# Kernel optimization log

Measured on AMD Instinct MI355X. Metric: run time of the kernel, lower is better.

Reference implementation:

```python
import math
import jax, jax.numpy as jnp
import numpy as np

V, D, H, L, F, T, B = 32000, 1024, 16, 4, 4096, 1024, 2
HD = D // H
EPS = 1e-5


def make_pe(max_len, d):
    pos = np.arange(max_len)[:, None].astype(np.float32)
    div = np.exp(np.arange(0, d, 2).astype(np.float32) * (-math.log(10000.0) / d))
    pe = np.zeros((max_len, d), dtype=np.float32)
    pe[:, 0::2] = np.sin(pos * div)
    pe[:, 1::2] = np.cos(pos * div)
    return jnp.asarray(pe)


def setup_inputs() -> dict:
    key = jax.random.key(0)
    ks = jax.random.split(key, 12)
    s = 0.02
    inp = {
        'tokens': jax.random.randint(ks[0], (B, T), 0, V, dtype=jnp.int32),
        'mask': jnp.tril(jnp.ones((T, T), dtype=jnp.int32)),
        'emb': jax.random.normal(ks[1], (V, D), jnp.float32) * s,
        'pe': make_pe(T, D),
        'ln1_g': jnp.ones((L, D)), 'ln1_b': jnp.zeros((L, D)),
        'Wqkv': jax.random.normal(ks[2], (L, D, 3 * D), jnp.float32) * s,
        'bqkv': jnp.zeros((L, 3 * D)),
        'Wproj': jax.random.normal(ks[3], (L, D, D), jnp.float32) * s,
        'bproj': jnp.zeros((L, D)),
        'ln2_g': jnp.ones((L, D)), 'ln2_b': jnp.zeros((L, D)),
        'W1': jax.random.normal(ks[4], (L, D, F), jnp.float32) * s,
        'b1': jnp.zeros((L, F)),
        'W2': jax.random.normal(ks[5], (L, F, D), jnp.float32) * s,
        'b2': jnp.zeros((L, D)),
        'lnf_g': jnp.ones((D,)), 'lnf_b': jnp.zeros((D,)),
        'out_b': jnp.zeros((V,)),
    }
    return inp


def layer_norm(x, g, b):
    m = jnp.mean(x, axis=-1, keepdims=True)
    v = jnp.mean((x - m) ** 2, axis=-1, keepdims=True)
    return (x - m) / jnp.sqrt(v + EPS) * g + b


def attention(x, mask, Wqkv, bqkv, Wproj, bproj):
    b, t, c = x.shape
    qkv = (x @ Wqkv + bqkv).reshape(b, t, 3, H, HD)
    q, k, v = jnp.moveaxis(qkv, 2, 0)  # each [B,T,H,HD]
    q = q.transpose(0, 2, 1, 3)  # [B,H,T,HD]
    k = k.transpose(0, 2, 1, 3)
    v = v.transpose(0, 2, 1, 3)
    scores = jnp.einsum('bhqd,bhkd->bhqk', q, k) / math.sqrt(HD)
    scores = jnp.where(mask[None, None] == 0, -1e9, scores)
    attn = jax.nn.softmax(scores, axis=-1)
    out = jnp.einsum('bhqk,bhkd->bhqd', attn, v)
    out = out.transpose(0, 2, 1, 3).reshape(b, t, c)
    return out @ Wproj + bproj, attn


def reference(tokens, mask, emb, pe, ln1_g, ln1_b, Wqkv, bqkv, Wproj, bproj,
              ln2_g, ln2_b, W1, b1, W2, b2, lnf_g, lnf_b, out_b):
    x = emb[tokens] + pe[:tokens.shape[1]]
    attn = None
    for i in range(L):
        a, attn = attention(layer_norm(x, ln1_g[i], ln1_b[i]), mask,
                            Wqkv[i], bqkv[i], Wproj[i], bproj[i])
        x = x + a
        h = layer_norm(x, ln2_g[i], ln2_b[i])
        h = jax.nn.gelu(h @ W1[i] + b1[i], approximate=False) @ W2[i] + b2[i]
        x = x + h
    x = layer_norm(x, lnf_g, lnf_b)
    logits = x @ emb.T + out_b  # weight tying
    return logits, attn
```

## Files before the change

kernel.cpp:

```cpp
#include <hip/hip_runtime.h>
#include <cstdint>

#define DEV static __device__ __forceinline__

typedef unsigned short u16;
typedef __bf16 bf16x8 __attribute__((ext_vector_type(8)));
typedef float f32x4 __attribute__((ext_vector_type(4)));
typedef unsigned short u16x4 __attribute__((ext_vector_type(4)));

constexpr int V = 32000, D = 1024, H = 16, L = 4, F = 4096, T = 1024, B = 2;
constexpr int HD = 64;

DEV u16 f2bf(float f) {
    union { float f; uint32_t i; } c; c.f = f;
    uint32_t x = c.i;
    return (u16)((x + 0x7fffu + ((x >> 16) & 1u)) >> 16);
}
DEV bf16x8 ld8(const u16* p) { return *reinterpret_cast<const bf16x8*>(p); }

DEV void gl16(const void* g, void* l) {
    __builtin_amdgcn_global_load_lds((const __attribute__((address_space(1))) void*)g,
                                     (__attribute__((address_space(3))) void*)l, 16, 0, 0);
}

__global__ __launch_bounds__(256) void k_embln(const int* __restrict__ tok,
        const float* __restrict__ emb, const float* __restrict__ pe,
        const float* __restrict__ g, const float* __restrict__ b,
        float* __restrict__ x, u16* __restrict__ out) {
    int row = blockIdx.x, tid = threadIdx.x;
    int t = row & (T - 1);
    int vv = tok[row];
    f32x4 v = ((const f32x4*)(emb + (size_t)vv * D))[tid] + ((const f32x4*)(pe + (size_t)t * D))[tid];
    ((f32x4*)(x + (size_t)row * D))[tid] = v;
    float s = v[0] + v[1] + v[2] + v[3];
    float s2 = v[0]*v[0] + v[1]*v[1] + v[2]*v[2] + v[3]*v[3];
#pragma unroll
    for (int m = 1; m < 64; m <<= 1) { s += __shfl_xor(s, m); s2 += __shfl_xor(s2, m); }
    __shared__ float ps[4], ps2[4];
    int wave = tid >> 6;
    if ((tid & 63) == 0) { ps[wave] = s; ps2[wave] = s2; }
    __syncthreads();
    s = ps[0] + ps[1] + ps[2] + ps[3];
    s2 = ps2[0] + ps2[1] + ps2[2] + ps2[3];
    float mean = s * (1.f / D);
    float var = s2 * (1.f / D) - mean * mean;
    float r = rsqrtf(var + 1e-5f);
    f32x4 gg = ((const f32x4*)g)[tid];
    f32x4 bb = ((const f32x4*)b)[tid];
    u16x4 o;
#pragma unroll
    for (int j = 0; j < 4; j++) o[j] = f2bf((v[j] - mean) * r * gg[j] + bb[j]);
    ((u16x4*)(out + (size_t)row * D))[tid] = o;
}

template <int S>
__global__ __launch_bounds__(256) void k_redln(const float* __restrict__ pp,
        const float* __restrict__ bias, float* __restrict__ x,
        const float* __restrict__ g, const float* __restrict__ b,
        u16* __restrict__ out) {
    int row = blockIdx.x, tid = threadIdx.x;
    f32x4 v = ((const f32x4*)(x + (size_t)row * D))[tid];
#pragma unroll
    for (int s = 0; s < S; s++)
        v += ((const f32x4*)(pp + ((size_t)s * (B * T) + row) * D))[tid];
    v += ((const f32x4*)bias)[tid];
    ((f32x4*)(x + (size_t)row * D))[tid] = v;
    float s = v[0] + v[1] + v[2] + v[3];
    float s2 = v[0]*v[0] + v[1]*v[1] + v[2]*v[2] + v[3]*v[3];
#pragma unroll
    for (int m = 1; m < 64; m <<= 1) { s += __shfl_xor(s, m); s2 += __shfl_xor(s2, m); }
    __shared__ float ps[4], ps2[4];
    int wave = tid >> 6;
    if ((tid & 63) == 0) { ps[wave] = s; ps2[wave] = s2; }
    __syncthreads();
    s = ps[0] + ps[1] + ps[2] + ps[3];
    s2 = ps2[0] + ps2[1] + ps2[2] + ps2[3];
    float mean = s * (1.f / D);
    float var = s2 * (1.f / D) - mean * mean;
    float r = rsqrtf(var + 1e-5f);
    f32x4 gg = ((const f32x4*)g)[tid];
    f32x4 bb = ((const f32x4*)b)[tid];
    u16x4 o;
#pragma unroll
    for (int j = 0; j < 4; j++) o[j] = f2bf((v[j] - mean) * r * gg[j] + bb[j]);
    ((u16x4*)(out + (size_t)row * D))[tid] = o;
}

__global__ __launch_bounds__(256) void k_cast(const float* __restrict__ src,
        u16* __restrict__ dst) {
    int i = (blockIdx.x * 256 + threadIdx.x) * 4;
    f32x4 v = *(const f32x4*)(src + i);
    u16x4 o;
#pragma unroll
    for (int j = 0; j < 4; j++) o[j] = f2bf(v[j]);
    *(u16x4*)(dst + i) = o;
}

__global__ __launch_bounds__(256) void k_castT4(const float* __restrict__ Wqkv,
        const float* __restrict__ Wproj, const float* __restrict__ W1,
        const float* __restrict__ W2, u16* __restrict__ wt) {
    int bid = blockIdx.x;
    const float* src; u16* dst; int Rr, Cc, t;
    if (bid < 3072)      { src = Wqkv;  dst = wt;                   Rr = D; Cc = 3 * D; t = bid; }
    else if (bid < 4096) { src = Wproj; dst = wt + 3 * D * D;       Rr = D; Cc = D;     t = bid - 3072; }
    else if (bid < 8192) { src = W1;    dst = wt + 4 * D * D;       Rr = D; Cc = F;     t = bid - 4096; }
    else                 { src = W2;    dst = wt + 4 * D * D + D * F; Rr = F; Cc = D;   t = bid - 8192; }
    int ntx = Cc >> 5;
    int c0 = (t % ntx) * 32, r0 = (t / ntx) * 32;
    __shared__ u16 tl[32][33];
    int x = threadIdx.x & 31, y = threadIdx.x >> 5;
#pragma unroll
    for (int i = 0; i < 4; i++)
        tl[y + i * 8][x] = f2bf(src[(size_t)(r0 + y + i * 8) * Cc + c0 + x]);
    __syncthreads();
#pragma unroll
    for (int i = 0; i < 4; i++)
        dst[(size_t)(c0 + y + i * 8) * Rr + r0 + x] = tl[x][y + i * 8];
}

template <int EPI, bool VT>
__global__ __launch_bounds__(256) void k_gemm_bt(
        const u16* __restrict__ A, int lda,
        const u16* __restrict__ Bt, int ldb,
        const float* __restrict__ bias,
        void* __restrict__ Cv, int ldc, int K, u16* __restrict__ vT) {
    __shared__ u16 tA[2][128 * 32];
    __shared__ u16 tB[2][128 * 32];
    int gm = gridDim.x;
    int nwg = gm * gridDim.y;
    int orig = blockIdx.y * gm + blockIdx.x;
    int xcd = orig & 7, idx = orig >> 3;
    int q = nwg >> 3, rr = nwg & 7;
    int wg = (xcd < rr ? xcd * (q + 1) : rr * (q + 1) + (xcd - rr) * q) + idx;
    int m0 = (wg % gm) * 128, n0 = (wg / gm) * 128;
    int koff = (EPI == 4) ? blockIdx.z * K : 0;
    int tid = threadIdx.x, wave = tid >> 6, lane = tid & 63;
    int llo = lane & 15, lhi = lane >> 4;
    int wr = wave >> 1, wc = wave & 1;
    f32x4 acc[4][4] = {};
    int nk = K / 32;
    for (int c = wave; c < 8; c += 4) {
        int e = (c * 64 + lane) * 8;
        int row = e >> 5, col = e & 31;
        gl16(A  + (size_t)(m0 + row) * lda + koff + col, &tA[0][c * 512]);
        gl16(Bt + (size_t)(n0 + row) * ldb + koff + col, &tB[0][c * 512]);
    }
    __syncthreads();
    int cur = 0;
    for (int t = 0; t < nk; ++t) {
        if (t + 1 < nk) {
            int kk = koff + (t + 1) * 32;
            for (int c = wave; c < 8; c += 4) {
                int e = (c * 64 + lane) * 8;
                int row = e >> 5, col = e & 31;
                gl16(A  + (size_t)(m0 + row) * lda + kk + col, &tA[cur ^ 1][c * 512]);
                gl16(Bt + (size_t)(n0 + row) * ldb + kk + col, &tB[cur ^ 1][c * 512]);
            }
        }
        bf16x8 af[4], bfr[4];
#pragma unroll
        for (int mi = 0; mi < 4; mi++) af[mi] = ld8(&tA[cur][(wr * 64 + mi * 16 + llo) * 32 + lhi * 8]);
#pragma unroll
        for (int ni = 0; ni < 4; ni++) bfr[ni] = ld8(&tB[cur][(wc * 64 + ni * 16 + llo) * 32 + lhi * 8]);
#pragma unroll
        for (int mi = 0; mi < 4; mi++)
#pragma unroll
            for (int ni = 0; ni < 4; ni++)
                acc[mi][ni] = __builtin_amdgcn_mfma_f32_16x16x32_bf16(af[mi], bfr[ni], acc[mi][ni], 0, 0, 0);
        __syncthreads();
        cur ^= 1;
    }
#pragma unroll
    for (int ni = 0; ni < 4; ni++) {
        int col = n0 + wc * 64 + ni * 16 + llo;
        float bb = 0.f;
        if (EPI != 4) bb = bias[col];
#pragma unroll
        for (int mi = 0; mi < 4; mi++) {
            int row0 = m0 + wr * 64 + mi * 16 + lhi * 4;
            if (VT && col >= 2 * D) {
                int dv = col - 2 * D;
                int b_ = row0 >> 10, t_ = row0 & (T - 1);
                u16x4 pk;
#pragma unroll
                for (int r = 0; r < 4; r++) pk[r] = f2bf(acc[mi][ni][r] + bb);
                *(u16x4*)(vT + ((size_t)(b_ * 16 + (dv >> 6)) * HD + (dv & 63)) * T + t_) = pk;
            } else {
#pragma unroll
                for (int r = 0; r < 4; r++) {
                    int row = row0 + r;
                    float o = acc[mi][ni][r] + bb;
                    if (EPI == 1) o = 0.5f * o * (1.f + erff(o * 0.70710678118f));
                    if (EPI == 3) {
                        ((float*)Cv)[(size_t)row * ldc + col] = o;
                    } else if (EPI == 4) {
                        ((float*)Cv)[((size_t)blockIdx.z * (B * T) + row) * ldc + col] = o;
                    } else {
                        ((u16*)Cv)[(size_t)row * ldc + col] = f2bf(o);
                    }
                }
            }
        }
    }
}

template <int PW>
__global__ __launch_bounds__(256) void k_fattn(const u16* __restrict__ qkv,
        const u16* __restrict__ vT, u16* __restrict__ out, float* __restrict__ attnF) {
    __shared__ u16 plds[4][16 * 40];
    int bh = blockIdx.y; int b = bh >> 4, h = bh & 15;
    int tid = threadIdx.x, wave = tid >> 6, lane = tid & 63;
    int llo = lane & 15, lhi = lane >> 4;
    int i0 = blockIdx.x * 64 + wave * 16;
    const u16* qb = qkv + (size_t)b * T * (3 * D) + h * HD;
    const u16* kb = qb + D;
    const u16* vt = vT + (size_t)bh * HD * T;
    bf16x8 q0 = ld8(qb + (size_t)(i0 + llo) * (3 * D) + lhi * 8);
    bf16x8 q1 = ld8(qb + (size_t)(i0 + llo) * (3 * D) + 32 + lhi * 8);
    int qrow = i0 + llo;
    float m = -3e38f, s = 0.f;
    f32x4 oacc[4] = {};
    u16* pw = &plds[wave][0];
    for (int k0 = 0; k0 < i0 + 16; k0 += 32) {
        f32x4 sc0 = {}, sc1 = {};
        {
            bf16x8 kf0 = ld8(kb + (size_t)(k0 + llo) * (3 * D) + lhi * 8);
            bf16x8 kf1 = ld8(kb + (size_t)(k0 + llo) * (3 * D) + 32 + lhi * 8);
            sc0 = __builtin_amdgcn_mfma_f32_16x16x32_bf16(kf0, q0, sc0, 0, 0, 0);
            sc0 = __builtin_amdgcn_mfma_f32_16x16x32_bf16(kf1, q1, sc0, 0, 0, 0);
        }
        if (k0 + 16 < i0 + 16) {
            bf16x8 kf0 = ld8(kb + (size_t)(k0 + 16 + llo) * (3 * D) + lhi * 8);
            bf16x8 kf1 = ld8(kb + (size_t)(k0 + 16 + llo) * (3 * D) + 32 + lhi * 8);
            sc1 = __builtin_amdgcn_mfma_f32_16x16x32_bf16(kf0, q0, sc1, 0, 0, 0);
            sc1 = __builtin_amdgcn_mfma_f32_16x16x32_bf16(kf1, q1, sc1, 0, 0, 0);
        }
        float vv[8]; float mx = m;
#pragma unroll
        for (int hf = 0; hf < 2; hf++)
#pragma unroll
            for (int r = 0; r < 4; r++) {
                int k = k0 + hf * 16 + lhi * 4 + r;
                float x = (hf ? sc1[r] : sc0[r]) * 0.125f;
                float v = (k <= qrow) ? x : -3e38f;
                vv[hf * 4 + r] = v;
                mx = fmaxf(mx, v);
            }
        mx = fmaxf(mx, __shfl_xor(mx, 16));
        mx = fmaxf(mx, __shfl_xor(mx, 32));
        float p[8]; float ps = 0.f;
#pragma unroll
        for (int j = 0; j < 8; j++) { p[j] = __expf(vv[j] - mx); ps += p[j]; }
        ps += __shfl_xor(ps, 16);
        ps += __shfl_xor(ps, 32);
        float scale = __expf(m - mx);
        s = s * scale + ps;
        m = mx;
        float sr[4];
#pragma unroll
        for (int r = 0; r < 4; r++) sr[r] = __shfl(scale, lhi * 4 + r);
#pragma unroll
        for (int n = 0; n < 4; n++)
#pragma unroll
            for (int r = 0; r < 4; r++) oacc[n][r] *= sr[r];
#pragma unroll
        for (int hf = 0; hf < 2; hf++) {
            u16x4 pk;
#pragma unroll
            for (int r = 0; r < 4; r++) pk[r] = f2bf(p[hf * 4 + r]);
            *(u16x4*)(pw + llo * 40 + hf * 16 + lhi * 4) = pk;
        }
        bf16x8 pa = ld8(pw + llo * 40 + lhi * 8);
#pragma unroll
        for (int n = 0; n < 4; n++) {
            bf16x8 vb = ld8(vt + (size_t)(n * 16 + llo) * T + k0 + lhi * 8);
            oacc[n] = __builtin_amdgcn_mfma_f32_16x16x32_bf16(pa, vb, oacc[n], 0, 0, 0);
        }
    }
    float inv = 1.f / s;
    float ir[4];
#pragma unroll
    for (int r = 0; r < 4; r++) ir[r] = __shfl(inv, lhi * 4 + r);
#pragma unroll
    for (int n = 0; n < 4; n++)
#pragma unroll
        for (int r = 0; r < 4; r++) {
            int i = i0 + lhi * 4 + r, c = n * 16 + llo;
            out[(size_t)(b * T + i) * D + h * HD + c] = f2bf(oacc[n][r] * ir[r]);
        }
    if (PW) {
        float* ar = attnF + ((size_t)bh * T + qrow) * T;
        for (int j0 = 0; j0 < T; j0 += 16) {
            f32x4 pv = {};
            if (j0 <= qrow) {
                if (j0 < i0 + 16) {
                    bf16x8 kf0 = ld8(kb + (size_t)(j0 + llo) * (3 * D) + lhi * 8);
                    bf16x8 kf1 = ld8(kb + (size_t)(j0 + llo) * (3 * D) + 32 + lhi * 8);
                    f32x4 sc = {};
                    sc = __builtin_amdgcn_mfma_f32_16x16x32_bf16(kf0, q0, sc, 0, 0, 0);
                    sc = __builtin_amdgcn_mfma_f32_16x16x32_bf16(kf1, q1, sc, 0, 0, 0);
#pragma unroll
                    for (int r = 0; r < 4; r++) {
                        int j = j0 + lhi * 4 + r;
                        pv[r] = (j <= qrow) ? __expf(sc[r] * 0.125f - m) * inv : 0.f;
                    }
                }
            }
            *(f32x4*)(ar + j0 + lhi * 4) = pv;
        }
    }
}

extern "C" void kernel_launch(void* const* d_in, const int* in_sizes, int n_in,
                              void* d_out, int out_size, void* d_ws, size_t ws_size,
                              hipStream_t stream) {
    const int*   tok   = (const int*)d_in[0];
    const float* emb   = (const float*)d_in[2];
    const float* pe    = (const float*)d_in[3];
    const float* ln1g  = (const float*)d_in[4];
    const float* ln1b  = (const float*)d_in[5];
    const float* Wqkv  = (const float*)d_in[6];
    const float* bqkv  = (const float*)d_in[7];
    const float* Wproj = (const float*)d_in[8];
    const float* bproj = (const float*)d_in[9];
    const float* ln2g  = (const float*)d_in[10];
    const float* ln2b  = (const float*)d_in[11];
    const float* W1    = (const float*)d_in[12];
    const float* b1    = (const float*)d_in[13];
    const float* W2    = (const float*)d_in[14];
    const float* b2    = (const float*)d_in[15];
    const float* lnfg  = (const float*)d_in[16];
    const float* lnfb  = (const float*)d_in[17];
    const float* outb  = (const float*)d_in[18];

    float* logits  = (float*)d_out;
    float* attnF   = logits + (size_t)B * T * V;

    char* w = (char*)d_ws;
    float* x    = (float*)w;  w += (size_t)B * T * D * 4;
    u16* lnout  = (u16*)w;    w += (size_t)B * T * D * 2;
    u16* qkv    = (u16*)w;    w += (size_t)B * T * 3 * D * 2;
    u16* vT     = (u16*)w;    w += (size_t)B * H * HD * T * 2;
    u16* aout   = (u16*)w;    w += (size_t)B * T * D * 2;
    char* tail = w;
    u16* hmid   = (u16*)w;    w += (size_t)B * T * F * 2;
    u16* WTL    = (u16*)w;    w += (size_t)(5 * D * D + 2 * D * F) * 2;
    float* pp   = (float*)w;  w += (size_t)4 * B * T * D * 4;
    u16* embB   = (u16*)tail;

    dim3 blk(256);
    k_embln<<<dim3(B * T), blk, 0, stream>>>(tok, emb, pe, ln1g, ln1b, x, lnout);

    for (int l = 0; l < L; l++) {
        k_castT4<<<dim3(12288), blk, 0, stream>>>(
            Wqkv + (size_t)l * D * 3 * D, Wproj + (size_t)l * D * D,
            W1 + (size_t)l * D * F, W2 + (size_t)l * F * D, WTL);
        k_gemm_bt<0, true><<<dim3(B * T / 128, 3 * D / 128), blk, 0, stream>>>(
            lnout, D, WTL, D, bqkv + l * 3 * D, qkv, 3 * D, D, vT);
        if (l == L - 1)
            k_fattn<1><<<dim3(T / 64, B * H), blk, 0, stream>>>(qkv, vT, aout, attnF);
        else
            k_fattn<0><<<dim3(T / 64, B * H), blk, 0, stream>>>(qkv, vT, aout, attnF);
        k_gemm_bt<4, false><<<dim3(B * T / 128, D / 128, 2), blk, 0, stream>>>(
            aout, D, WTL + (size_t)3 * D * D, D, nullptr, pp, D, D / 2, nullptr);
        k_redln<2><<<dim3(B * T), blk, 0, stream>>>(pp, bproj + l * D, x,
            ln2g + l * D, ln2b + l * D, lnout);
        k_gemm_bt<1, false><<<dim3(B * T / 128, F / 128), blk, 0, stream>>>(
            lnout, D, WTL + (size_t)4 * D * D, D, b1 + l * F, hmid, F, D, nullptr);
        k_gemm_bt<4, false><<<dim3(B * T / 128, D / 128, 4), blk, 0, stream>>>(
            hmid, F, WTL + (size_t)4 * D * D + D * F, F, nullptr, pp, D, F / 4, nullptr);
        const float* ng = (l == L - 1) ? lnfg : ln1g + (l + 1) * D;
        const float* nb = (l == L - 1) ? lnfb : ln1b + (l + 1) * D;
        k_redln<4><<<dim3(B * T), blk, 0, stream>>>(pp, b2 + l * D, x, ng, nb, lnout);
    }
    k_cast<<<dim3(V * D / 1024), blk, 0, stream>>>(emb, embB);
    k_gemm_bt<3, false><<<dim3(B * T / 128, V / 128), blk, 0, stream>>>(
        lnout, D, embB, D, outb, logits, V, D, nullptr);
}
```

Measured before the change: 1.101 ms.

## Add 256x256 eight-wave pipelined GEMM for output logits projection

```diff
diff --git a/kernel.cpp b/kernel.cpp
--- a/kernel.cpp
+++ b/kernel.cpp
@@ -204,6 +204,122 @@
     }
 }
 
+DEV bf16x8 ldf(const u16* half, int row, int lhi) {
+    int lb = row * 64 + lhi * 16;
+    lb ^= ((lb >> 9) & 1) << 5;
+    return *(const bf16x8*)((const char*)half + lb);
+}
+DEV void stg(const u16* gb, int ld, int kc, u16* dstBase, int wave, int lane) {
+#pragma unroll
+    for (int i = 0; i < 2; i++) {
+        int p = (wave * 2 + i) * 64 + lane;
+        int l = p ^ (((p >> 5) & 1) << 1);
+        gl16(gb + (size_t)(l >> 2) * ld + kc + (l & 3) * 8, dstBase + (wave * 2 + i) * 512);
+    }
+}
+#define SB_BAR() do { __builtin_amdgcn_sched_barrier(0); __builtin_amdgcn_s_barrier(); } while (0)
+
+__global__ __launch_bounds__(512, 2) void k_gemm8(
+        const u16* __restrict__ A, int lda,
+        const u16* __restrict__ Bt, int ldb,
+        const float* __restrict__ bias,
+        float* __restrict__ C, int ldc, int K) {
+    __shared__ u16 lds[2][4][256 * 32];
+    int gm = gridDim.x, nwg = gm * gridDim.y;
+    int orig = blockIdx.y * gm + blockIdx.x;
+    int xcd = orig & 7, idx = orig >> 3;
+    int q = nwg >> 3, rr = nwg & 7;
+    int wg = (xcd < rr ? xcd * (q + 1) : rr * (q + 1) + (xcd - rr) * q) + idx;
+    int m0 = (wg % gm) * 256, n0 = (wg / gm) * 256;
+    int tid = threadIdx.x, wave = tid >> 6, lane = tid & 63;
+    int llo = lane & 15, lhi = lane >> 4;
+    int wm = wave >> 2, wn = wave & 3;
+    const u16* Ab = A + (size_t)m0 * lda;
+    const u16* Bb = Bt + (size_t)n0 * ldb;
+    int nk = K >> 6;
+    f32x4 acc[8][4] = {};
+    stg(Ab, lda, 0,   &lds[0][0][0], wave, lane);
+    stg(Bb, ldb, 0,   &lds[0][1][0], wave, lane);
+    stg(Ab, lda, 32,  &lds[0][2][0], wave, lane);
+    stg(Bb, ldb, 32,  &lds[0][3][0], wave, lane);
+    stg(Ab, lda, 64,  &lds[1][0][0], wave, lane);
+    stg(Bb, ldb, 64,  &lds[1][1][0], wave, lane);
+    stg(Ab, lda, 96,  &lds[1][2][0], wave, lane);
+    asm volatile("s_waitcnt vmcnt(10)");
+    SB_BAR();
+    for (int t = 0; t < nk; ++t) {
+        const int bf = t & 1;
+        bf16x8 af[8], b0, b1;
+#pragma unroll
+        for (int mi = 0; mi < 8; mi++) af[mi] = ldf(&lds[bf][0][0], wm * 128 + mi * 16 + llo, lhi);
+        b0 = ldf(&lds[bf][1][0], wn * 64 + llo, lhi);
+        b1 = ldf(&lds[bf][1][0], wn * 64 + 16 + llo, lhi);
+        if (t + 1 < nk) stg(Bb, ldb, (t + 1) * 64 + 32, &lds[bf ^ 1][3][0], wave, lane);
+        __builtin_amdgcn_s_setprio(1);
+#pragma unroll
+        for (int mi = 0; mi < 8; mi++) {
+            acc[mi][0] = __builtin_amdgcn_mfma_f32_16x16x32_bf16(af[mi], b0, acc[mi][0], 0, 0, 0);
+            acc[mi][1] = __builtin_amdgcn_mfma_f32_16x16x32_bf16(af[mi], b1, acc[mi][1], 0, 0, 0);
+        }
+        __builtin_amdgcn_s_setprio(0);
+        SB_BAR();
+        b0 = ldf(&lds[bf][1][0], wn * 64 + 32 + llo, lhi);
+        b1 = ldf(&lds[bf][1][0], wn * 64 + 48 + llo, lhi);
+        if (t + 2 < nk) stg(Ab, lda, (t + 2) * 64, &lds[bf][0][0], wave, lane);
+        __builtin_amdgcn_s_setprio(1);
+#pragma unroll
+        for (int mi = 0; mi < 8; mi++) {
+            acc[mi][2] = __builtin_amdgcn_mfma_f32_16x16x32_bf16(af[mi], b0, acc[mi][2], 0, 0, 0);
+            acc[mi][3] = __builtin_amdgcn_mfma_f32_16x16x32_bf16(af[mi], b1, acc[mi][3], 0, 0, 0);
+        }
+        __builtin_amdgcn_s_setprio(0);
+        if (t + 2 < nk)      { asm volatile("s_waitcnt vmcnt(10)"); }
+        else if (t + 1 < nk) { asm volatile("s_waitcnt vmcnt(8)"); }
+        else                 { asm volatile("s_waitcnt vmcnt(0)"); }
+        SB_BAR();
+#pragma unroll
+        for (int mi = 0; mi < 8; mi++) af[mi] = ldf(&lds[bf][2][0], wm * 128 + mi * 16 + llo, lhi);
+        b0 = ldf(&lds[bf][3][0], wn * 64 + llo, lhi);
+        b1 = ldf(&lds[bf][3][0], wn * 64 + 16 + llo, lhi);
+        if (t + 2 < nk) stg(Bb, ldb, (t + 2) * 64, &lds[bf][1][0], wave, lane);
+        __builtin_amdgcn_s_setprio(1);
+#pragma unroll
+        for (int mi = 0; mi < 8; mi++) {
+            acc[mi][0] = __builtin_amdgcn_mfma_f32_16x16x32_bf16(af[mi], b0, acc[mi][0], 0, 0, 0);
+            acc[mi][1] = __builtin_amdgcn_mfma_f32_16x16x32_bf16(af[mi], b1, acc[mi][1], 0, 0, 0);
+        }
+        __builtin_amdgcn_s_setprio(0);
+        SB_BAR();
+        b0 = ldf(&lds[bf][3][0], wn * 64 + 32 + llo, lhi);
+        b1 = ldf(&lds[bf][3][0], wn * 64 + 48 + llo, lhi);
+        if (t + 2 < nk) stg(Ab, lda, (t + 2) * 64 + 32, &lds[bf][2][0], wave, lane);
+        __builtin_amdgcn_s_setprio(1);
+#pragma unroll
+        for (int mi = 0; mi < 8; mi++) {
+            acc[mi][2] = __builtin_amdgcn_mfma_f32_16x16x32_bf16(af[mi], b0, acc[mi][2], 0, 0, 0);
+            acc[mi][3] = __builtin_amdgcn_mfma_f32_16x16x32_bf16(af[mi], b1, acc[mi][3], 0, 0, 0);
+        }
+        __builtin_amdgcn_s_setprio(0);
+        if (t + 1 < nk) {
+            if (t + 2 < nk) { asm volatile("s_waitcnt vmcnt(10)"); }
+            else            { asm volatile("s_waitcnt vmcnt(4)"); }
+        }
+        SB_BAR();
+    }
+#pragma unroll
+    for (int ni = 0; ni < 4; ni++) {
+        int col = n0 + wn * 64 + ni * 16 + llo;
+        float bb = bias[col];
+#pragma unroll
+        for (int mi = 0; mi < 8; mi++) {
+            int row0 = m0 + wm * 128 + mi * 16 + lhi * 4;
+#pragma unroll
+            for (int r = 0; r < 4; r++)
+                C[(size_t)(row0 + r) * ldc + col] = acc[mi][ni][r] + bb;
+        }
+    }
+}
+
 template <int PW>
 __global__ __launch_bounds__(256) void k_fattn(const u16* __restrict__ qkv,
         const u16* __restrict__ vT, u16* __restrict__ out, float* __restrict__ attnF) {
@@ -374,6 +490,6 @@
         k_redln<4><<<dim3(B * T), blk, 0, stream>>>(pp, b2 + l * D, x, ng, nb, lnout);
     }
     k_cast<<<dim3(V * D / 1024), blk, 0, stream>>>(emb, embB);
-    k_gemm_bt<3, false><<<dim3(B * T / 128, V / 128), blk, 0, stream>>>(
-        lnout, D, embB, D, outb, logits, V, D, nullptr);
-}
+    k_gemm8<<<dim3(B * T / 256, V / 256), dim3(512), 0, stream>>>(
+        lnout, D, embB, D, outb, logits, V, D);
+}
```

After: 1.069 ms. 1.03x faster.
